# Kernel optimization log

Measured on AMD Instinct MI355X. Metric: run time of the kernel, lower is better.

The kernel has to match this reference:

```python
import jax, jax.numpy as jnp
import numpy as np

B, T, D, HS = 4, 4096, 512, 64


def setup_inputs() -> dict:
    key = jax.random.key(0)
    kx, kd, kk, kq, kv = jax.random.split(key, 5)
    X = jax.random.normal(kx, (B, T, D), dtype=jnp.float32)
    dag = jax.random.randint(kd, (T, T), 0, 2, dtype=jnp.int32)
    scale = 1.0 / np.sqrt(D).astype(np.float32)
    Wk = jax.random.normal(kk, (D, HS), dtype=jnp.float32) * scale
    Wq = jax.random.normal(kq, (D, HS), dtype=jnp.float32) * scale
    Wv = jax.random.normal(kv, (D, HS), dtype=jnp.float32) * scale
    return {"X": X, "dag": dag, "Wk": Wk, "Wq": Wq, "Wv": Wv}


def reference(X, dag, Wk, Wq, Wv):
    # Projections (nn.Linear without bias): [B,T,HS]
    K = X @ Wk
    Q = X @ Wq
    V = X @ Wv
    hs = Q.shape[-1]
    # Dense scores [B,T,T]
    QK = jnp.einsum('bid,bjd->bij', Q, K) / np.float32(np.sqrt(hs))
    mask = (dag == 0)  # [T,T], True -> -inf
    # Rows fully masked would softmax to NaN in torch; the module zeroes them.
    row_dead = jnp.all(mask, axis=-1)  # [T]
    neg_inf = jnp.asarray(-jnp.inf, QK.dtype)
    scores = jnp.where(mask, neg_inf, QK)
    # Neutralize dead rows before softmax to avoid NaN, then zero them out
    scores = jnp.where(row_dead[:, None], jnp.zeros((), QK.dtype), scores)
    att = jax.nn.softmax(scores, axis=-1)
    att = jnp.where(row_dead[:, None], jnp.zeros((), att.dtype), att)
    # Transposed AV matmul: out[b,j,h] = sum_i att[b,i,j] * V[b,i,h]
    out = jnp.einsum('bij,bih->bjh', att, V)
    # Swish activation
    return out * jax.nn.sigmoid(out)
```

## Files before the change

kernel.cpp:

```cpp
#include <hip/hip_runtime.h>
#include <hip/hip_bf16.h>
#include <math.h>

#define BB 4
#define TT 4096
#define DD 512
#define HH 64
#define TW 128

typedef unsigned int u32;
typedef unsigned short u16;
typedef float f32x16 __attribute__((ext_vector_type(16)));
typedef __bf16 bf16x8 __attribute__((ext_vector_type(8)));

#define SC 0.18033688011112042f

static __device__ __forceinline__ u16 f2b(float f) {
    __hip_bfloat16 h = __float2bfloat16(f);
    return __builtin_bit_cast(u16, h);
}
static __device__ __forceinline__ float b2f(u16 x) {
    return __builtin_bit_cast(float, (u32)x << 16);
}
static __device__ __forceinline__ u32 pk2(float a, float b) {
    return (u32)f2b(a) | ((u32)f2b(b) << 16);
}
static __device__ __forceinline__ bf16x8 ldf(const u16* p) {
    uint4 u = *(const uint4*)p;
    return __builtin_bit_cast(bf16x8, u);
}
static __device__ __forceinline__ void swap32(u32& a, u32& b) {
    asm("v_permlane32_swap_b32 %0, %1" : "+v"(a), "+v"(b));
}


__global__ __launch_bounds__(256) void pack_kernel(const int* __restrict__ dag,
                                                   u32* __restrict__ bits2,
                                                   u32* __restrict__ bitsTT,
                                                   const float* __restrict__ Wq,
                                                   const float* __restrict__ Wk,
                                                   const float* __restrict__ Wv,
                                                   u16* __restrict__ Wt) {
    if (blockIdx.x >= 2048) {
        const int wb = blockIdx.x - 2048;
        const int m = wb >> 3, sub = wb & 7;
        const float* W = (m == 0) ? Wq : (m == 1) ? Wk : Wv;
        const int t = threadIdx.x;
        const int n = sub * 8 + (t >> 5);
        const int k0 = (t & 31) * 16;
        u16 buf[16];
#pragma unroll
        for (int k = 0; k < 16; ++k) buf[k] = f2b(W[(size_t)(k0 + k) * HH + n]);
        uint4* dst = (uint4*)(Wt + ((size_t)m * 64 + n) * DD + k0);
        dst[0] = *(uint4*)buf;
        dst[1] = *(uint4*)(buf + 8);
        return;
    }
    const int unit = blockIdx.x * 4 + (threadIdx.x >> 6);
    const int lane = threadIdx.x & 63;
    const int i64 = unit >> 7;
    const int j32 = unit & 127;
    const int i = i64 * 64 + lane;
    const int* p = dag + (size_t)i * TT + j32 * 32;
    u32 rw = 0;
#pragma unroll
    for (int c = 0; c < 32; c += 4) {
        int4 v = *(const int4*)(p + c);
        rw |= (v.x != 0 ? 1u : 0u) << c;
        rw |= (v.y != 0 ? 1u : 0u) << (c + 1);
        rw |= (v.z != 0 ? 1u : 0u) << (c + 2);
        rw |= (v.w != 0 ? 1u : 0u) << (c + 3);
    }
    bits2[(size_t)j32 * TT + i] = rw;
    u32 myw = 0;
#pragma unroll
    for (int c = 0; c < 32; ++c) {
        unsigned long long m = __ballot((rw >> c) & 1);
        u32 part = (lane < 32) ? (u32)m : (u32)(m >> 32);
        if ((lane & 31) == c) myw = part;
    }
    bitsTT[(size_t)(i64 * 2 + (lane >> 5)) * TT + j32 * 32 + (lane & 31)] = myw;
}

__global__ __launch_bounds__(384) void proj_kernel(const float* __restrict__ X,
                                                   const u16* __restrict__ Wt,
                                                   u16* __restrict__ QF,
                                                   u16* __restrict__ KF,
                                                   u16* __restrict__ VF) {
    const int w = threadIdx.x >> 6, lane = threadIdx.x & 63;
    const int m = w % 3, rg = w / 3;
    const int l31 = lane & 31, hf = lane >> 5;
    const int tile = blockIdx.x * 2 + rg;
    const int row0 = tile * 32;
    const float* xr = X + (size_t)(row0 + l31) * DD + hf * 8;
    const u16* wbase = Wt + (size_t)m * 64 * DD + hf * 8;

    f32x16 acc[2] = {};

    for (int kt = 0; kt < 32; ++kt) {
        float4 x0 = *(const float4*)(xr + kt * 16);
        float4 x1 = *(const float4*)(xr + kt * 16 + 4);
        uint4 aw;
        aw.x = pk2(x0.x, x0.y);
        aw.y = pk2(x0.z, x0.w);
        aw.z = pk2(x1.x, x1.y);
        aw.w = pk2(x1.z, x1.w);
        bf16x8 xa = __builtin_bit_cast(bf16x8, aw);
        const u16* wk = wbase + kt * 16;
#pragma unroll
        for (int nt = 0; nt < 2; ++nt) {
            bf16x8 wb = ldf(wk + (size_t)(nt * 32 + l31) * DD);
            acc[nt] = __builtin_amdgcn_mfma_f32_32x32x16_bf16(xa, wb, acc[nt], 0, 0, 0);
        }
    }
    const float sc = (m == 0) ? SC : 1.0f;
    if (m < 2) {
        u16* dst = (m == 0) ? QF : KF;
        const int kth = l31 >> 4, hfp = (l31 >> 3) & 1, e = l31 & 7;
#pragma unroll
        for (int nt = 0; nt < 2; ++nt)
#pragma unroll
            for (int r = 0; r < 16; ++r) {
                int rl = (r & 3) + 8 * (r >> 2) + 4 * hf;
                dst[(size_t)tile * 2048 + (nt * 2 + kth) * 512 + (rl + hfp * 32) * 8 + e]
                    = f2b(acc[nt][r] * sc);
            }
    } else {
#pragma unroll
        for (int nt = 0; nt < 2; ++nt)
#pragma unroll
            for (int r = 0; r < 16; ++r) {
                int rl = (r & 3) + 8 * (r >> 2) + 4 * hf;
                VF[(size_t)tile * 2048 + (nt * 2 + (rl >> 4)) * 512
                   + (l31 + ((rl >> 3) & 1) * 32) * 8 + (rl & 7)] = f2b(acc[nt][r]);
            }
    }
}

__global__ __launch_bounds__(512, 4) void stats_kernel(const u16* __restrict__ QF,
                                                       const u16* __restrict__ KF,
                                                       const u32* __restrict__ bits2,
                                                       float* __restrict__ cOut) {
    __shared__ float Lsh[8][64];
    const int bid = blockIdx.x;
    const int b = (bid & 7) >> 1;
    const int itg = (bid & 1) * 64 + (bid >> 3);
    const int i0 = itg * 32;
    const int w = threadIdx.x >> 6, lane = threadIdx.x & 63;
    const int l31 = lane & 31, hf = lane >> 5;

    bf16x8 qf[4];
    const u16* qbase = QF + (size_t)(b * 128 + itg) * 2048 + lane * 8;
#pragma unroll
    for (int kt = 0; kt < 4; ++kt) qf[kt] = ldf(qbase + kt * 512);

    const u16* kf0 = KF + (size_t)b * 128 * 2048 + lane * 8;

    float Lp = 0.f;
    for (int t = 0; t < 16; ++t) {
        const int jt = w + t * 8;
        const u16* kb = kf0 + (size_t)jt * 2048;
        u32 mw = bits2[(size_t)jt * TT + i0 + l31];

        __builtin_amdgcn_s_setprio(1);
        f32x16 s = {};
        s = __builtin_amdgcn_mfma_f32_32x32x16_bf16(ldf(kb), qf[0], s, 0, 0, 0);
        s = __builtin_amdgcn_mfma_f32_32x32x16_bf16(ldf(kb + 512), qf[1], s, 0, 0, 0);
        s = __builtin_amdgcn_mfma_f32_32x32x16_bf16(ldf(kb + 1024), qf[2], s, 0, 0, 0);
        s = __builtin_amdgcn_mfma_f32_32x32x16_bf16(ldf(kb + 1536), qf[3], s, 0, 0, 0);
        __builtin_amdgcn_s_setprio(0);
        u32 mwr = __builtin_amdgcn_alignbit(mw, mw, hf * 4);
#pragma unroll
        for (int r = 0; r < 16; ++r) {
            const int pos = (r & 3) + 8 * (r >> 2);
            float e = __builtin_amdgcn_exp2f(s[r]);
            Lp += ((mwr >> pos) & 1) ? e : 0.f;
        }
    }
    Lsh[w][lane] = Lp;
    __syncthreads();
    if (threadIdx.x < 32) {
        const int il = threadIdx.x;
        float L = 0.f;
#pragma unroll
        for (int q = 0; q < 8; ++q) L += Lsh[q][il] + Lsh[q][il + 32];
        cOut[(size_t)b * TT + i0 + il] = (L > 0.f) ? 1.f / L : 0.f;
    }
}

__global__ __launch_bounds__(256) void scalev_kernel(const u16* __restrict__ VF,
                                                     const float* __restrict__ cB,
                                                     u16* __restrict__ VF2) {
    const int bid = blockIdx.x;
    const int b = (bid & 7) >> 1;
    const int itg = (bid & 1) * 64 + (bid >> 3);
    const int tile = b * 128 + itg;
    const int q = threadIdx.x >> 6, ln = threadIdx.x & 63;
    const float* c = cB + (size_t)b * TT + itg * 32 + (q & 1) * 16 + (ln >> 5) * 8;
    float4 c0 = *(const float4*)c;
    float4 c1 = *(const float4*)(c + 4);
    const u16* p = VF + (size_t)tile * 2048 + q * 512 + ln * 8;
    uint4 v = *(const uint4*)p;
    u16* ve = (u16*)&v;
    ve[0] = f2b(b2f(ve[0]) * c0.x);
    ve[1] = f2b(b2f(ve[1]) * c0.y);
    ve[2] = f2b(b2f(ve[2]) * c0.z);
    ve[3] = f2b(b2f(ve[3]) * c0.w);
    ve[4] = f2b(b2f(ve[4]) * c1.x);
    ve[5] = f2b(b2f(ve[5]) * c1.y);
    ve[6] = f2b(b2f(ve[6]) * c1.z);
    ve[7] = f2b(b2f(ve[7]) * c1.w);
    *(uint4*)(VF2 + (size_t)tile * 2048 + q * 512 + ln * 8) = v;
}

__global__ __launch_bounds__(512, 4) void out_kernel(const u16* __restrict__ QF,
                                                     const u16* __restrict__ KF,
                                                     const u16* __restrict__ VF2,
                                                     const u32* __restrict__ bitsTT,
                                                     float* __restrict__ out) {
    __shared__ float red[4][2048];
    const int bid = blockIdx.x;
    const int b = (bid & 7) >> 1;
    const int jt = (bid & 1) * 64 + (bid >> 3);
    const int j0 = jt * 32;
    const int w = threadIdx.x >> 6, lane = threadIdx.x & 63;
    const int l31 = lane & 31, hf = lane >> 5;

    bf16x8 kf[4];
    const u16* kbase = KF + (size_t)(b * 128 + jt) * 2048 + lane * 8;
#pragma unroll
    for (int kt = 0; kt < 4; ++kt) kf[kt] = ldf(kbase + kt * 512);

    const u16* qf0 = QF + (size_t)b * 128 * 2048 + lane * 8;
    const u16* vf0 = VF2 + (size_t)b * 128 * 2048 + lane * 8;

    f32x16 acc0 = {}, acc1 = {};

    for (int t = 0; t < 16; ++t) {
        const int it = w + t * 8;
        const u16* qb = qf0 + (size_t)it * 2048;
        const u16* vb = vf0 + (size_t)it * 2048;
        u32 mw = bitsTT[(size_t)it * TT + j0 + l31];

        __builtin_amdgcn_s_setprio(1);
        f32x16 s = {};
        s = __builtin_amdgcn_mfma_f32_32x32x16_bf16(ldf(qb), kf[0], s, 0, 0, 0);
        s = __builtin_amdgcn_mfma_f32_32x32x16_bf16(ldf(qb + 512), kf[1], s, 0, 0, 0);
        s = __builtin_amdgcn_mfma_f32_32x32x16_bf16(ldf(qb + 1024), kf[2], s, 0, 0, 0);
        s = __builtin_amdgcn_mfma_f32_32x32x16_bf16(ldf(qb + 1536), kf[3], s, 0, 0, 0);
        __builtin_amdgcn_s_setprio(0);

        u32 mwr = __builtin_amdgcn_alignbit(mw, mw, hf * 4);

        float p[16];
#pragma unroll
        for (int r = 0; r < 16; ++r) {
            const int pos = (r & 3) + 8 * (r >> 2);
            float e = __builtin_amdgcn_exp2f(s[r]);
            p[r] = ((mwr >> pos) & 1) ? e : 0.f;
        }

        {
            u32 a  = pk2(p[0], p[1]);
            u32 bq = pk2(p[2], p[3]);
            u32 c  = pk2(p[4], p[5]);
            u32 d  = pk2(p[6], p[7]);
            swap32(a, c);
            swap32(bq, d);
            uint4 aww = {a, bq, c, d};
            bf16x8 pa = __builtin_bit_cast(bf16x8, aww);
            __builtin_amdgcn_s_setprio(1);
            acc0 = __builtin_amdgcn_mfma_f32_32x32x16_bf16(pa, ldf(vb), acc0, 0, 0, 0);
            acc1 = __builtin_amdgcn_mfma_f32_32x32x16_bf16(pa, ldf(vb + 1024), acc1, 0, 0, 0);
            __builtin_amdgcn_s_setprio(0);
        }
        {
            u32 a  = pk2(p[8], p[9]);
            u32 bq = pk2(p[10], p[11]);
            u32 c  = pk2(p[12], p[13]);
            u32 d  = pk2(p[14], p[15]);
            swap32(a, c);
            swap32(bq, d);
            uint4 aww = {a, bq, c, d};
            bf16x8 pa = __builtin_bit_cast(bf16x8, aww);
            __builtin_amdgcn_s_setprio(1);
            acc0 = __builtin_amdgcn_mfma_f32_32x32x16_bf16(pa, ldf(vb + 512), acc0, 0, 0, 0);
            acc1 = __builtin_amdgcn_mfma_f32_32x32x16_bf16(pa, ldf(vb + 1536), acc1, 0, 0, 0);
            __builtin_amdgcn_s_setprio(0);
        }
    }

    if (w >= 4) {
        float* myred = &red[w - 4][0];
#pragma unroll
        for (int r = 0; r < 16; ++r) {
            int jl = (r & 3) + 8 * (r >> 2) + 4 * hf;
            myred[jl * 64 + l31] = acc0[r];
            myred[jl * 64 + 32 + l31] = acc1[r];
        }
    }
    __syncthreads();
    if (w < 4) {
        float* myred = &red[w][0];
#pragma unroll
        for (int r = 0; r < 16; ++r) {
            int jl = (r & 3) + 8 * (r >> 2) + 4 * hf;
            acc0[r] += myred[jl * 64 + l31];
            acc1[r] += myred[jl * 64 + 32 + l31];
        }
#pragma unroll
        for (int r = 0; r < 16; ++r) {
            int jl = (r & 3) + 8 * (r >> 2) + 4 * hf;
            myred[jl * 64 + l31] = acc0[r];
            myred[jl * 64 + 32 + l31] = acc1[r];
        }
    }
    __syncthreads();
    {
        const int tid = threadIdx.x;
        float4 r0 = *(const float4*)&red[0][tid * 4];
        float4 r1 = *(const float4*)&red[1][tid * 4];
        float4 r2 = *(const float4*)&red[2][tid * 4];
        float4 r3 = *(const float4*)&red[3][tid * 4];
        float v0 = r0.x + r1.x + r2.x + r3.x;
        float v1 = r0.y + r1.y + r2.y + r3.y;
        float v2 = r0.z + r1.z + r2.z + r3.z;
        float v3 = r0.w + r1.w + r2.w + r3.w;
        v0 = v0 / (1.f + __expf(-v0));
        v1 = v1 / (1.f + __expf(-v1));
        v2 = v2 / (1.f + __expf(-v2));
        v3 = v3 / (1.f + __expf(-v3));
        const int jl = tid >> 4, hc = (tid * 4) & 63;
        float* dst = out + ((size_t)b * TT + j0 + jl) * HH + hc;
        *(float4*)dst = make_float4(v0, v1, v2, v3);
    }
}

extern "C" void kernel_launch(void* const* d_in, const int* in_sizes, int n_in,
                              void* d_out, int out_size, void* d_ws, size_t ws_size,
                              hipStream_t stream) {
    const float* X  = (const float*)d_in[0];
    const int*  dag = (const int*)d_in[1];
    const float* Wk = (const float*)d_in[2];
    const float* Wq = (const float*)d_in[3];
    const float* Wv = (const float*)d_in[4];
    float* out = (float*)d_out;

    char* ws = (char*)d_ws;
    u16*   QF    = (u16*)ws;
    u16*   KF    = (u16*)(ws + (2u << 20));
    u16*   VF    = (u16*)(ws + (4u << 20));
    u16*   VF2   = (u16*)(ws + (6u << 20));
    u32*   bits2 = (u32*)(ws + (8u << 20));
    u32*   bitsTT= (u32*)(ws + (10u << 20));
    u16*   Wt    = (u16*)(ws + (12u << 20));
    float* cB    = (float*)(ws + (12u << 20) + (256u << 10));

    pack_kernel<<<2048 + 24, 256, 0, stream>>>(dag, bits2, bitsTT, Wq, Wk, Wv, Wt);
    proj_kernel<<<256, 384, 0, stream>>>(X, Wt, QF, KF, VF);
    stats_kernel<<<512, 512, 0, stream>>>(QF, KF, bits2, cB);
    scalev_kernel<<<512, 256, 0, stream>>>(VF, cB, VF2);
    out_kernel<<<512, 512, 0, stream>>>(QF, KF, VF2, bitsTT, out);
}
```

Measured before the change: 96.67 us.

## Fold softmax normalizer into score MFMA as log-bias, drop scalev kernel

```diff
diff --git a/kernel.cpp b/kernel.cpp
--- a/kernel.cpp
+++ b/kernel.cpp
@@ -27,6 +27,9 @@
 }
 static __device__ __forceinline__ bf16x8 ldf(const u16* p) {
     uint4 u = *(const uint4*)p;
+    return __builtin_bit_cast(bf16x8, u);
+}
+static __device__ __forceinline__ bf16x8 c8(uint4 u) {
     return __builtin_bit_cast(bf16x8, u);
 }
 static __device__ __forceinline__ void swap32(u32& a, u32& b) {
@@ -140,7 +143,7 @@
 __global__ __launch_bounds__(512, 4) void stats_kernel(const u16* __restrict__ QF,
                                                        const u16* __restrict__ KF,
                                                        const u32* __restrict__ bits2,
-                                                       float* __restrict__ cOut) {
+                                                       float* __restrict__ lcOut) {
     __shared__ float Lsh[8][64];
     const int bid = blockIdx.x;
     const int b = (bid & 7) >> 1;
@@ -184,39 +187,15 @@
         float L = 0.f;
 #pragma unroll
         for (int q = 0; q < 8; ++q) L += Lsh[q][il] + Lsh[q][il + 32];
-        cOut[(size_t)b * TT + i0 + il] = (L > 0.f) ? 1.f / L : 0.f;
-    }
-}
-
-__global__ __launch_bounds__(256) void scalev_kernel(const u16* __restrict__ VF,
-                                                     const float* __restrict__ cB,
-                                                     u16* __restrict__ VF2) {
-    const int bid = blockIdx.x;
-    const int b = (bid & 7) >> 1;
-    const int itg = (bid & 1) * 64 + (bid >> 3);
-    const int tile = b * 128 + itg;
-    const int q = threadIdx.x >> 6, ln = threadIdx.x & 63;
-    const float* c = cB + (size_t)b * TT + itg * 32 + (q & 1) * 16 + (ln >> 5) * 8;
-    float4 c0 = *(const float4*)c;
-    float4 c1 = *(const float4*)(c + 4);
-    const u16* p = VF + (size_t)tile * 2048 + q * 512 + ln * 8;
-    uint4 v = *(const uint4*)p;
-    u16* ve = (u16*)&v;
-    ve[0] = f2b(b2f(ve[0]) * c0.x);
-    ve[1] = f2b(b2f(ve[1]) * c0.y);
-    ve[2] = f2b(b2f(ve[2]) * c0.z);
-    ve[3] = f2b(b2f(ve[3]) * c0.w);
-    ve[4] = f2b(b2f(ve[4]) * c1.x);
-    ve[5] = f2b(b2f(ve[5]) * c1.y);
-    ve[6] = f2b(b2f(ve[6]) * c1.z);
-    ve[7] = f2b(b2f(ve[7]) * c1.w);
-    *(uint4*)(VF2 + (size_t)tile * 2048 + q * 512 + ln * 8) = v;
+        lcOut[(size_t)b * TT + i0 + il] = (L > 0.f) ? -__log2f(L) : -30000.0f;
+    }
 }
 
 __global__ __launch_bounds__(512, 4) void out_kernel(const u16* __restrict__ QF,
                                                      const u16* __restrict__ KF,
-                                                     const u16* __restrict__ VF2,
+                                                     const u16* __restrict__ VF,
                                                      const u32* __restrict__ bitsTT,
+                                                     const float* __restrict__ lcB,
                                                      float* __restrict__ out) {
     __shared__ float red[4][2048];
     const int bid = blockIdx.x;
@@ -232,7 +211,10 @@
     for (int kt = 0; kt < 4; ++kt) kf[kt] = ldf(kbase + kt * 512);
 
     const u16* qf0 = QF + (size_t)b * 128 * 2048 + lane * 8;
-    const u16* vf0 = VF2 + (size_t)b * 128 * 2048 + lane * 8;
+    const u16* vf0 = VF + (size_t)b * 128 * 2048 + lane * 8;
+    const float* lc0 = lcB + (size_t)b * TT;
+
+    const uint4 oneB = {hf ? 0u : 0x3F803F80u, 0u, 0u, 0u};
 
     f32x16 acc0 = {}, acc1 = {};
 
@@ -242,8 +224,15 @@
         const u16* vb = vf0 + (size_t)it * 2048;
         u32 mw = bitsTT[(size_t)it * TT + j0 + l31];
 
+        float lcv = lc0[it * 32 + l31];
+        u16 lch = f2b(lcv);
+        float lcl = lcv - b2f(lch);
+        u32 lcw = (u32)lch | ((u32)f2b(lcl) << 16);
+        uint4 lcA = {hf ? 0u : lcw, 0u, 0u, 0u};
+
         __builtin_amdgcn_s_setprio(1);
         f32x16 s = {};
+        s = __builtin_amdgcn_mfma_f32_32x32x16_bf16(c8(lcA), c8(oneB), s, 0, 0, 0);
         s = __builtin_amdgcn_mfma_f32_32x32x16_bf16(ldf(qb), kf[0], s, 0, 0, 0);
         s = __builtin_amdgcn_mfma_f32_32x32x16_bf16(ldf(qb + 512), kf[1], s, 0, 0, 0);
         s = __builtin_amdgcn_mfma_f32_32x32x16_bf16(ldf(qb + 1024), kf[2], s, 0, 0, 0);
@@ -350,15 +339,13 @@
     u16*   QF    = (u16*)ws;
     u16*   KF    = (u16*)(ws + (2u << 20));
     u16*   VF    = (u16*)(ws + (4u << 20));
-    u16*   VF2   = (u16*)(ws + (6u << 20));
-    u32*   bits2 = (u32*)(ws + (8u << 20));
-    u32*   bitsTT= (u32*)(ws + (10u << 20));
-    u16*   Wt    = (u16*)(ws + (12u << 20));
-    float* cB    = (float*)(ws + (12u << 20) + (256u << 10));
+    u32*   bits2 = (u32*)(ws + (6u << 20));
+    u32*   bitsTT= (u32*)(ws + (8u << 20));
+    u16*   Wt    = (u16*)(ws + (10u << 20));
+    float* lcB   = (float*)(ws + (10u << 20) + (256u << 10));
 
     pack_kernel<<<2048 + 24, 256, 0, stream>>>(dag, bits2, bitsTT, Wq, Wk, Wv, Wt);
     proj_kernel<<<256, 384, 0, stream>>>(X, Wt, QF, KF, VF);
-    stats_kernel<<<512, 512, 0, stream>>>(QF, KF, bits2, cB);
-    scalev_kernel<<<512, 256, 0, stream>>>(VF, cB, VF2);
-    out_kernel<<<512, 512, 0, stream>>>(QF, KF, VF2, bitsTT, out);
-}
+    stats_kernel<<<512, 512, 0, stream>>>(QF, KF, bits2, lcB);
+    out_kernel<<<512, 512, 0, stream>>>(QF, KF, VF, bitsTT, lcB, out);
+}
```

Result: no change. 98.36 us (+1.8%).

## Process two query/key tiles per block to reuse streamed K/Q/V fragments

Applied to the files above, without the earlier changes.

```diff
diff --git a/kernel.cpp b/kernel.cpp
--- a/kernel.cpp
+++ b/kernel.cpp
@@ -27,6 +27,9 @@
 }
 static __device__ __forceinline__ bf16x8 ldf(const u16* p) {
     uint4 u = *(const uint4*)p;
+    return __builtin_bit_cast(bf16x8, u);
+}
+static __device__ __forceinline__ bf16x8 c8(uint4 u) {
     return __builtin_bit_cast(bf16x8, u);
 }
 static __device__ __forceinline__ void swap32(u32& a, u32& b) {
@@ -137,54 +140,68 @@
     }
 }
 
-__global__ __launch_bounds__(512, 4) void stats_kernel(const u16* __restrict__ QF,
+__global__ __launch_bounds__(512, 2) void stats_kernel(const u16* __restrict__ QF,
                                                        const u16* __restrict__ KF,
                                                        const u32* __restrict__ bits2,
                                                        float* __restrict__ cOut) {
-    __shared__ float Lsh[8][64];
+    __shared__ float Lsh[8][128];
     const int bid = blockIdx.x;
     const int b = (bid & 7) >> 1;
-    const int itg = (bid & 1) * 64 + (bid >> 3);
-    const int i0 = itg * 32;
+    const int u = (bid & 1) * 32 + (bid >> 3);
+    const int itg0 = u * 2;
+    const int i0 = itg0 * 32;
     const int w = threadIdx.x >> 6, lane = threadIdx.x & 63;
     const int l31 = lane & 31, hf = lane >> 5;
 
-    bf16x8 qf[4];
-    const u16* qbase = QF + (size_t)(b * 128 + itg) * 2048 + lane * 8;
-#pragma unroll
-    for (int kt = 0; kt < 4; ++kt) qf[kt] = ldf(qbase + kt * 512);
+    bf16x8 qfA[4], qfB[4];
+    const u16* qbase = QF + (size_t)(b * 128 + itg0) * 2048 + lane * 8;
+#pragma unroll
+    for (int kt = 0; kt < 4; ++kt) {
+        qfA[kt] = ldf(qbase + kt * 512);
+        qfB[kt] = ldf(qbase + 2048 + kt * 512);
+    }
 
     const u16* kf0 = KF + (size_t)b * 128 * 2048 + lane * 8;
 
-    float Lp = 0.f;
+    float LpA = 0.f, LpB = 0.f;
     for (int t = 0; t < 16; ++t) {
         const int jt = w + t * 8;
         const u16* kb = kf0 + (size_t)jt * 2048;
-        u32 mw = bits2[(size_t)jt * TT + i0 + l31];
-
+        u32 mwA = bits2[(size_t)jt * TT + i0 + l31];
+        u32 mwB = bits2[(size_t)jt * TT + i0 + 32 + l31];
+
+        bf16x8 k0 = ldf(kb), k1 = ldf(kb + 512), k2 = ldf(kb + 1024), k3 = ldf(kb + 1536);
         __builtin_amdgcn_s_setprio(1);
-        f32x16 s = {};
-        s = __builtin_amdgcn_mfma_f32_32x32x16_bf16(ldf(kb), qf[0], s, 0, 0, 0);
-        s = __builtin_amdgcn_mfma_f32_32x32x16_bf16(ldf(kb + 512), qf[1], s, 0, 0, 0);
-        s = __builtin_amdgcn_mfma_f32_32x32x16_bf16(ldf(kb + 1024), qf[2], s, 0, 0, 0);
-        s = __builtin_amdgcn_mfma_f32_32x32x16_bf16(ldf(kb + 1536), qf[3], s, 0, 0, 0);
+        f32x16 sA = {}, sB = {};
+        sA = __builtin_amdgcn_mfma_f32_32x32x16_bf16(k0, qfA[0], sA, 0, 0, 0);
+        sB = __builtin_amdgcn_mfma_f32_32x32x16_bf16(k0, qfB[0], sB, 0, 0, 0);
+        sA = __builtin_amdgcn_mfma_f32_32x32x16_bf16(k1, qfA[1], sA, 0, 0, 0);
+        sB = __builtin_amdgcn_mfma_f32_32x32x16_bf16(k1, qfB[1], sB, 0, 0, 0);
+        sA = __builtin_amdgcn_mfma_f32_32x32x16_bf16(k2, qfA[2], sA, 0, 0, 0);
+        sB = __builtin_amdgcn_mfma_f32_32x32x16_bf16(k2, qfB[2], sB, 0, 0, 0);
+        sA = __builtin_amdgcn_mfma_f32_32x32x16_bf16(k3, qfA[3], sA, 0, 0, 0);
+        sB = __builtin_amdgcn_mfma_f32_32x32x16_bf16(k3, qfB[3], sB, 0, 0, 0);
         __builtin_amdgcn_s_setprio(0);
-        u32 mwr = __builtin_amdgcn_alignbit(mw, mw, hf * 4);
+        u32 mrA = __builtin_amdgcn_alignbit(mwA, mwA, hf * 4);
+        u32 mrB = __builtin_amdgcn_alignbit(mwB, mwB, hf * 4);
 #pragma unroll
         for (int r = 0; r < 16; ++r) {
             const int pos = (r & 3) + 8 * (r >> 2);
-            float e = __builtin_amdgcn_exp2f(s[r]);
-            Lp += ((mwr >> pos) & 1) ? e : 0.f;
-        }
-    }
-    Lsh[w][lane] = Lp;
+            float eA = __builtin_amdgcn_exp2f(sA[r]);
+            float eB = __builtin_amdgcn_exp2f(sB[r]);
+            LpA += ((mrA >> pos) & 1) ? eA : 0.f;
+            LpB += ((mrB >> pos) & 1) ? eB : 0.f;
+        }
+    }
+    Lsh[w][lane] = LpA;
+    Lsh[w][64 + lane] = LpB;
     __syncthreads();
-    if (threadIdx.x < 32) {
-        const int il = threadIdx.x;
+    if (threadIdx.x < 64) {
+        const int g = threadIdx.x >> 5, il = threadIdx.x & 31;
         float L = 0.f;
 #pragma unroll
-        for (int q = 0; q < 8; ++q) L += Lsh[q][il] + Lsh[q][il + 32];
-        cOut[(size_t)b * TT + i0 + il] = (L > 0.f) ? 1.f / L : 0.f;
+        for (int q = 0; q < 8; ++q) L += Lsh[q][g * 64 + il] + Lsh[q][g * 64 + il + 32];
+        cOut[(size_t)b * TT + i0 + g * 32 + il] = (L > 0.f) ? 1.f / L : 0.f;
     }
 }
 
@@ -213,126 +230,133 @@
     *(uint4*)(VF2 + (size_t)tile * 2048 + q * 512 + ln * 8) = v;
 }
 
-__global__ __launch_bounds__(512, 4) void out_kernel(const u16* __restrict__ QF,
+__global__ __launch_bounds__(512, 2) void out_kernel(const u16* __restrict__ QF,
                                                      const u16* __restrict__ KF,
                                                      const u16* __restrict__ VF2,
                                                      const u32* __restrict__ bitsTT,
                                                      float* __restrict__ out) {
-    __shared__ float red[4][2048];
+    __shared__ float red[2][4][2048];
     const int bid = blockIdx.x;
     const int b = (bid & 7) >> 1;
-    const int jt = (bid & 1) * 64 + (bid >> 3);
-    const int j0 = jt * 32;
+    const int u = (bid & 1) * 32 + (bid >> 3);
+    const int jt0 = u * 2;
+    const int j0 = jt0 * 32;
     const int w = threadIdx.x >> 6, lane = threadIdx.x & 63;
     const int l31 = lane & 31, hf = lane >> 5;
 
-    bf16x8 kf[4];
-    const u16* kbase = KF + (size_t)(b * 128 + jt) * 2048 + lane * 8;
-#pragma unroll
-    for (int kt = 0; kt < 4; ++kt) kf[kt] = ldf(kbase + kt * 512);
+    bf16x8 kfA[4], kfB[4];
+    const u16* kbase = KF + (size_t)(b * 128 + jt0) * 2048 + lane * 8;
+#pragma unroll
+    for (int kt = 0; kt < 4; ++kt) {
+        kfA[kt] = ldf(kbase + kt * 512);
+        kfB[kt] = ldf(kbase + 2048 + kt * 512);
+    }
 
     const u16* qf0 = QF + (size_t)b * 128 * 2048 + lane * 8;
     const u16* vf0 = VF2 + (size_t)b * 128 * 2048 + lane * 8;
 
-    f32x16 acc0 = {}, acc1 = {};
+    f32x16 accA0 = {}, accA1 = {}, accB0 = {}, accB1 = {};
 
     for (int t = 0; t < 16; ++t) {
         const int it = w + t * 8;
         const u16* qb = qf0 + (size_t)it * 2048;
         const u16* vb = vf0 + (size_t)it * 2048;
-        u32 mw = bitsTT[(size_t)it * TT + j0 + l31];
-
+        u32 mwA = bitsTT[(size_t)it * TT + j0 + l31];
+        u32 mwB = bitsTT[(size_t)it * TT + j0 + 32 + l31];
+
+        bf16x8 q0 = ldf(qb), q1 = ldf(qb + 512), q2 = ldf(qb + 1024), q3 = ldf(qb + 1536);
         __builtin_amdgcn_s_setprio(1);
-        f32x16 s = {};
-        s = __builtin_amdgcn_mfma_f32_32x32x16_bf16(ldf(qb), kf[0], s, 0, 0, 0);
-        s = __builtin_amdgcn_mfma_f32_32x32x16_bf16(ldf(qb + 512), kf[1], s, 0, 0, 0);
-        s = __builtin_amdgcn_mfma_f32_32x32x16_bf16(ldf(qb + 1024), kf[2], s, 0, 0, 0);
-        s = __builtin_amdgcn_mfma_f32_32x32x16_bf16(ldf(qb + 1536), kf[3], s, 0, 0, 0);
+        f32x16 sA = {}, sB = {};
+        sA = __builtin_amdgcn_mfma_f32_32x32x16_bf16(q0, kfA[0], sA, 0, 0, 0);
+        sB = __builtin_amdgcn_mfma_f32_32x32x16_bf16(q0, kfB[0], sB, 0, 0, 0);
+        sA = __builtin_amdgcn_mfma_f32_32x32x16_bf16(q1, kfA[1], sA, 0, 0, 0);
+        sB = __builtin_amdgcn_mfma_f32_32x32x16_bf16(q1, kfB[1], sB, 0, 0, 0);
+        sA = __builtin_amdgcn_mfma_f32_32x32x16_bf16(q2, kfA[2], sA, 0, 0, 0);
+        sB = __builtin_amdgcn_mfma_f32_32x32x16_bf16(q2, kfB[2], sB, 0, 0, 0);
+        sA = __builtin_amdgcn_mfma_f32_32x32x16_bf16(q3, kfA[3], sA, 0, 0, 0);
+        sB = __builtin_amdgcn_mfma_f32_32x32x16_bf16(q3, kfB[3], sB, 0, 0, 0);
         __builtin_amdgcn_s_setprio(0);
 
-        u32 mwr = __builtin_amdgcn_alignbit(mw, mw, hf * 4);
-
-        float p[16];
+        u32 mrA = __builtin_amdgcn_alignbit(mwA, mwA, hf * 4);
+        u32 mrB = __builtin_amdgcn_alignbit(mwB, mwB, hf * 4);
+
+        float pA[16], pB[16];
 #pragma unroll
         for (int r = 0; r < 16; ++r) {
             const int pos = (r & 3) + 8 * (r >> 2);
-            float e = __builtin_amdgcn_exp2f(s[r]);
-            p[r] = ((mwr >> pos) & 1) ? e : 0.f;
-        }
-
-        {
-            u32 a  = pk2(p[0], p[1]);
-            u32 bq = pk2(p[2], p[3]);
-            u32 c  = pk2(p[4], p[5]);
-            u32 d  = pk2(p[6], p[7]);
-            swap32(a, c);
-            swap32(bq, d);
-            uint4 aww = {a, bq, c, d};
-            bf16x8 pa = __builtin_bit_cast(bf16x8, aww);
+            float eA = __builtin_amdgcn_exp2f(sA[r]);
+            float eB = __builtin_amdgcn_exp2f(sB[r]);
+            pA[r] = ((mrA >> pos) & 1) ? eA : 0.f;
+            pB[r] = ((mrB >> pos) & 1) ? eB : 0.f;
+        }
+
+        bf16x8 v00 = ldf(vb), v01 = ldf(vb + 512), v10 = ldf(vb + 1024), v11 = ldf(vb + 1536);
+
+#pragma unroll
+        for (int k2 = 0; k2 < 2; ++k2) {
+            u32 aA  = pk2(pA[8 * k2 + 0], pA[8 * k2 + 1]);
+            u32 bA  = pk2(pA[8 * k2 + 2], pA[8 * k2 + 3]);
+            u32 cA  = pk2(pA[8 * k2 + 4], pA[8 * k2 + 5]);
+            u32 dA  = pk2(pA[8 * k2 + 6], pA[8 * k2 + 7]);
+            swap32(aA, cA);
+            swap32(bA, dA);
+            uint4 awA = {aA, bA, cA, dA};
+            bf16x8 paA = __builtin_bit_cast(bf16x8, awA);
+            u32 aB  = pk2(pB[8 * k2 + 0], pB[8 * k2 + 1]);
+            u32 bB  = pk2(pB[8 * k2 + 2], pB[8 * k2 + 3]);
+            u32 cB2 = pk2(pB[8 * k2 + 4], pB[8 * k2 + 5]);
+            u32 dB  = pk2(pB[8 * k2 + 6], pB[8 * k2 + 7]);
+            swap32(aB, cB2);
+            swap32(bB, dB);
+            uint4 awB = {aB, bB, cB2, dB};
+            bf16x8 paB = __builtin_bit_cast(bf16x8, awB);
+            bf16x8 v0 = (k2 == 0) ? v00 : v01;
+            bf16x8 v1 = (k2 == 0) ? v10 : v11;
             __builtin_amdgcn_s_setprio(1);
-            acc0 = __builtin_amdgcn_mfma_f32_32x32x16_bf16(pa, ldf(vb), acc0, 0, 0, 0);
-            acc1 = __builtin_amdgcn_mfma_f32_32x32x16_bf16(pa, ldf(vb + 1024), acc1, 0, 0, 0);
+            accA0 = __builtin_amdgcn_mfma_f32_32x32x16_bf16(paA, v0, accA0, 0, 0, 0);
+            accB0 = __builtin_amdgcn_mfma_f32_32x32x16_bf16(paB, v0, accB0, 0, 0, 0);
+            accA1 = __builtin_amdgcn_mfma_f32_32x32x16_bf16(paA, v1, accA1, 0, 0, 0);
+            accB1 = __builtin_amdgcn_mfma_f32_32x32x16_bf16(paB, v1, accB1, 0, 0, 0);
             __builtin_amdgcn_s_setprio(0);
         }
-        {
-            u32 a  = pk2(p[8], p[9]);
-            u32 bq = pk2(p[10], p[11]);
-            u32 c  = pk2(p[12], p[13]);
-            u32 d  = pk2(p[14], p[15]);
-            swap32(a, c);
-            swap32(bq, d);
-            uint4 aww = {a, bq, c, d};
-            bf16x8 pa = __builtin_bit_cast(bf16x8, aww);
-            __builtin_amdgcn_s_setprio(1);
-            acc0 = __builtin_amdgcn_mfma_f32_32x32x16_bf16(pa, ldf(vb + 512), acc0, 0, 0, 0);
-            acc1 = __builtin_amdgcn_mfma_f32_32x32x16_bf16(pa, ldf(vb + 1536), acc1, 0, 0, 0);
-            __builtin_amdgcn_s_setprio(0);
-        }
     }
 
     if (w >= 4) {
-        float* myred = &red[w - 4][0];
 #pragma unroll
         for (int r = 0; r < 16; ++r) {
             int jl = (r & 3) + 8 * (r >> 2) + 4 * hf;
-            myred[jl * 64 + l31] = acc0[r];
-            myred[jl * 64 + 32 + l31] = acc1[r];
+            red[0][w - 4][jl * 64 + l31] = accA0[r];
+            red[0][w - 4][jl * 64 + 32 + l31] = accA1[r];
+            red[1][w - 4][jl * 64 + l31] = accB0[r];
+            red[1][w - 4][jl * 64 + 32 + l31] = accB1[r];
         }
     }
     __syncthreads();
     if (w < 4) {
-        float* myred = &red[w][0];
 #pragma unroll
         for (int r = 0; r < 16; ++r) {
             int jl = (r & 3) + 8 * (r >> 2) + 4 * hf;
-            acc0[r] += myred[jl * 64 + l31];
-            acc1[r] += myred[jl * 64 + 32 + l31];
-        }
-#pragma unroll
-        for (int r = 0; r < 16; ++r) {
-            int jl = (r & 3) + 8 * (r >> 2) + 4 * hf;
-            myred[jl * 64 + l31] = acc0[r];
-            myred[jl * 64 + 32 + l31] = acc1[r];
+            red[0][w][jl * 64 + l31] += accA0[r];
+            red[0][w][jl * 64 + 32 + l31] += accA1[r];
+            red[1][w][jl * 64 + l31] += accB0[r];
+            red[1][w][jl * 64 + 32 + l31] += accB1[r];
         }
     }
     __syncthreads();
     {
-        const int tid = threadIdx.x;
-        float4 r0 = *(const float4*)&red[0][tid * 4];
-        float4 r1 = *(const float4*)&red[1][tid * 4];
-        float4 r2 = *(const float4*)&red[2][tid * 4];
-        float4 r3 = *(const float4*)&red[3][tid * 4];
-        float v0 = r0.x + r1.x + r2.x + r3.x;
-        float v1 = r0.y + r1.y + r2.y + r3.y;
-        float v2 = r0.z + r1.z + r2.z + r3.z;
-        float v3 = r0.w + r1.w + r2.w + r3.w;
-        v0 = v0 / (1.f + __expf(-v0));
-        v1 = v1 / (1.f + __expf(-v1));
-        v2 = v2 / (1.f + __expf(-v2));
-        v3 = v3 / (1.f + __expf(-v3));
-        const int jl = tid >> 4, hc = (tid * 4) & 63;
-        float* dst = out + ((size_t)b * TT + j0 + jl) * HH + hc;
-        *(float4*)dst = make_float4(v0, v1, v2, v3);
+        const int idx = threadIdx.x * 8;
+        const int g3 = idx >> 11, e = idx & 2047;
+        float vv[8];
+#pragma unroll
+        for (int q = 0; q < 8; ++q) {
+            int ee = e + q;
+            float v = red[g3][0][ee] + red[g3][1][ee] + red[g3][2][ee] + red[g3][3][ee];
+            vv[q] = v / (1.f + __expf(-v));
+        }
+        const int jl = e >> 6, hc = e & 63;
+        float* dst = out + ((size_t)b * TT + (jt0 + g3) * 32 + jl) * HH + hc;
+        *(float4*)dst = make_float4(vv[0], vv[1], vv[2], vv[3]);
+        *(float4*)(dst + 4) = make_float4(vv[4], vv[5], vv[6], vv[7]);
     }
 }
 
@@ -358,7 +382,7 @@
 
     pack_kernel<<<2048 + 24, 256, 0, stream>>>(dag, bits2, bitsTT, Wq, Wk, Wv, Wt);
     proj_kernel<<<256, 384, 0, stream>>>(X, Wt, QF, KF, VF);
-    stats_kernel<<<512, 512, 0, stream>>>(QF, KF, bits2, cB);
+    stats_kernel<<<256, 512, 0, stream>>>(QF, KF, bits2, cB);
     scalev_kernel<<<512, 256, 0, stream>>>(VF, cB, VF2);
-    out_kernel<<<512, 512, 0, stream>>>(QF, KF, VF2, bitsTT, out);
-}
+    out_kernel<<<256, 512, 0, stream>>>(QF, KF, VF2, bitsTT, out);
+}
```

Result: faster. 94.52 us (-2.2%).
